# Kernel optimization log

Measured on AMD Instinct MI355X. Metric: run time of the kernel, lower is better.

Reference implementation:

```python
import jax, jax.numpy as jnp
import numpy as np

B, C, T_TEXT, T_FEAT = 32, 256, 512, 2048
DELTA = 0.1  # self.temperature


def setup_inputs() -> dict:
    key = jax.random.key(0)
    k1, k2 = jax.random.split(key)
    x = jax.random.normal(k1, (B, C, T_TEXT), dtype=jnp.float32)
    # token durations in frames, ~U[0, 8): avg ~4 frames/token -> T_FEAT ~ 2048
    w = jax.random.uniform(k2, (B, T_TEXT), dtype=jnp.float32) * 8.0
    x_mask = jnp.ones((B, T_TEXT), dtype=bool)
    y_mask = jnp.ones((B, T_FEAT), dtype=bool)
    return {"x": x, "w": w, "x_mask": x_mask, "y_mask": y_mask}


def reference(x, w, x_mask, y_mask):
    # Gaussian upsampling (arXiv 2010.04301) with fixed temperature DELTA.
    # x: (B, C, T_text), w: (B, T_text), x_mask: (B, T_text), y_mask: (B, T_feat)
    T_feats = y_mask.shape[-1]
    # frame time indices, zeroed where y_mask is False
    t = jnp.arange(T_feats, dtype=jnp.float32)[None, :] * y_mask.astype(jnp.float32)  # (B, T_feat)
    # Gaussian centers: cumulative duration minus half of own duration
    c = jnp.cumsum(w, axis=-1) - 0.5 * w  # (B, T_text)
    # energy: -delta * (t - c)^2  -> (B, T_feat, T_text)
    energy = -DELTA * (t[:, :, None] - c[:, None, :]) ** 2
    # mask out padded text tokens
    energy = jnp.where(x_mask[:, None, :], energy, -jnp.inf)
    p_attn = jax.nn.softmax(energy, axis=-1)  # (B, T_feat, T_text)
    # weighted sum over text tokens: (B, C, T_feat)
    out = jnp.einsum("btn,bcn->bct", p_attn, x)
    return out
```

## Files before the change

### kernel.cpp

```cpp
#include <hip/hip_runtime.h>
#include <hip/hip_bf16.h>

#define B_    32
#define C_    256
#define NT    512
#define TFEAT 2048
#define TT    32
#define UW    96
#define PRE   32
#define DELTA 0.1f
#define PSTR  104

typedef __attribute__((ext_vector_type(4))) float f32x4;
typedef __attribute__((ext_vector_type(8))) unsigned short u16x8;
typedef __attribute__((ext_vector_type(8))) __bf16 bf16x8;

static __device__ inline unsigned short f2bfbits(float f) {
    __bf16 h = (__bf16)f;
    return __builtin_bit_cast(unsigned short, h);
}
static __device__ inline float bf2f(unsigned short h) {
    return __uint_as_float(((unsigned)h) << 16);
}

__global__ __launch_bounds__(512) void centers_kernel(const float* __restrict__ w,
                                                      float* __restrict__ cout,
                                                      int* __restrict__ lotab) {
    int b = blockIdx.x;
    int tid = threadIdx.x;
    int lane = tid & 63, wv = tid >> 6;
    __shared__ float wsum[8];
    __shared__ float cs[NT];

    float wval = w[b * NT + tid];
    float s = wval;
#pragma unroll
    for (int off = 1; off < 64; off <<= 1) {
        float v = __shfl_up(s, off);
        if (lane >= off) s += v;
    }
    if (lane == 63) wsum[wv] = s;
    __syncthreads();
    float base = 0.f;
#pragma unroll
    for (int i = 0; i < 8; ++i) base += (i < wv) ? wsum[i] : 0.f;
    float c = base + s - 0.5f * wval;
    cs[tid] = c;
    cout[b * NT + tid] = c;
    __syncthreads();

    if (tid < TFEAT / TT) {
        float ft = (float)(tid * TT);
        int lo = 0, hi = NT;
        while (hi > lo) {
            int mid = (lo + hi) >> 1;
            if (cs[mid] < ft) lo = mid + 1; else hi = mid;
        }
        int n1 = lo < NT - 1 ? lo : NT - 1;
        int n0 = lo - 1 > 0 ? lo - 1 : 0;
        int nstar = (fabsf(ft - cs[n0]) <= fabsf(ft - cs[n1])) ? n0 : n1;
        int L = (nstar - PRE) & ~3;
        if (L < 0) L = 0;
        if (L > NT - UW) L = NT - UW;
        lotab[b * (TFEAT / TT) + tid] = L;
    }
}

__global__ __launch_bounds__(256) void fused_kernel(const float* __restrict__ x,
                                                    const float* __restrict__ cw,
                                                    const int* __restrict__ lotab,
                                                    float* __restrict__ out) {
    __shared__ unsigned short Pt[TT][PSTR];
    __shared__ float Sinv[TT];

    int tid = threadIdx.x;
    int bx  = blockIdx.x;
    int b    = bx & 31;
    int tile = bx >> 5;
    int t0   = tile * TT;
    int LO   = lotab[b * (TFEAT / TT) + tile];

    int wv   = tid >> 6;
    int lane = tid & 63;
    int arow = lane & 15;
    int kg   = lane >> 4;
    const float* xb = x + ((size_t)b * C_) * NT + LO + kg * 8;
    f32x4 areg[12][2];
#pragma unroll
    for (int m = 0; m < 4; ++m) {
        const float* xr = xb + (size_t)(wv * 64 + m * 16 + arow) * NT;
#pragma unroll
        for (int ks = 0; ks < 3; ++ks) {
            areg[m * 3 + ks][0] = *reinterpret_cast<const f32x4*>(xr + ks * 32);
            areg[m * 3 + ks][1] = *reinterpret_cast<const f32x4*>(xr + ks * 32 + 4);
        }
    }

    int g = tid >> 3;
    int j = tid & 7;
    float ft = (float)(t0 + g);

    float csv[12];
    const float* cp = cw + b * NT + LO + j;
#pragma unroll
    for (int k = 0; k < 12; ++k) csv[k] = cp[8 * k];

    float e[12];
    float mx = -1e30f;
#pragma unroll
    for (int k = 0; k < 12; ++k) {
        float d = ft - csv[k];
        e[k] = -DELTA * d * d;
        mx = fmaxf(mx, e[k]);
    }
    mx = fmaxf(mx, __shfl_xor(mx, 1));
    mx = fmaxf(mx, __shfl_xor(mx, 2));
    mx = fmaxf(mx, __shfl_xor(mx, 4));

    float sum = 0.f;
#pragma unroll
    for (int k = 0; k < 12; ++k) {
        unsigned short pb = f2bfbits(__expf(e[k] - mx));
        sum += bf2f(pb);
        Pt[g][j + 8 * k] = pb;
    }
    sum += __shfl_xor(sum, 1);
    sum += __shfl_xor(sum, 2);
    sum += __shfl_xor(sum, 4);
    if (j == 0) Sinv[g] = 1.f / fmaxf(sum, 1e-30f);

    bf16x8 afrag[12];
#pragma unroll
    for (int f = 0; f < 12; ++f) {
        bf16x8 v;
#pragma unroll
        for (int q = 0; q < 4; ++q) {
            v[q]     = (__bf16)areg[f][0][q];
            v[q + 4] = (__bf16)areg[f][1][q];
        }
        afrag[f] = v;
    }
    __syncthreads();

    bf16x8 bfrag[6];
#pragma unroll
    for (int nt = 0; nt < 2; ++nt)
#pragma unroll
        for (int ks = 0; ks < 3; ++ks) {
            const u16x8* p = reinterpret_cast<const u16x8*>(
                &Pt[nt * 16 + (lane & 15)][ks * 32 + kg * 8]);
            bfrag[nt * 3 + ks] = __builtin_bit_cast(bf16x8, *p);
        }

    f32x4 acc[4][2];
#pragma unroll
    for (int m = 0; m < 4; ++m)
#pragma unroll
        for (int nt = 0; nt < 2; ++nt)
            acc[m][nt] = (f32x4){0.f, 0.f, 0.f, 0.f};
#pragma unroll
    for (int m = 0; m < 4; ++m)
#pragma unroll
        for (int nt = 0; nt < 2; ++nt)
#pragma unroll
            for (int ks = 0; ks < 3; ++ks)
                acc[m][nt] = __builtin_amdgcn_mfma_f32_16x16x32_bf16(
                    afrag[m * 3 + ks], bfrag[nt * 3 + ks], acc[m][nt], 0, 0, 0);

    float si0 = Sinv[lane & 15];
    float si1 = Sinv[16 + (lane & 15)];
    int orow = (lane >> 4) * 4;
    float* ob = out + ((size_t)b * C_) * TFEAT + t0;
#pragma unroll
    for (int m = 0; m < 4; ++m) {
        int c = wv * 64 + m * 16 + orow;
#pragma unroll
        for (int r = 0; r < 4; ++r) {
            __builtin_nontemporal_store(acc[m][0][r] * si0,
                ob + (size_t)(c + r) * TFEAT + (lane & 15));
            __builtin_nontemporal_store(acc[m][1][r] * si1,
                ob + (size_t)(c + r) * TFEAT + 16 + (lane & 15));
        }
    }
}

extern "C" void kernel_launch(void* const* d_in, const int* in_sizes, int n_in,
                              void* d_out, int out_size, void* d_ws, size_t ws_size,
                              hipStream_t stream) {
    const float* x = (const float*)d_in[0];
    const float* w = (const float*)d_in[1];
    float* out  = (float*)d_out;
    float* cbuf = (float*)d_ws;
    int*   lotab = (int*)((char*)d_ws + 65536);

    hipLaunchKernelGGL(centers_kernel, dim3(B_), dim3(NT), 0, stream, w, cbuf, lotab);
    hipLaunchKernelGGL(fused_kernel, dim3(B_ * (TFEAT / TT)), dim3(256), 0, stream,
                       x, cbuf, lotab, out);
}
```

Baseline: 35.95 us.

## Fuse centers computation into main kernel and pipeline four tiles per block

Removes the separate centers/lotab kernel. Each block now recomputes the cumulative-sum centers for its batch in shared memory and finds the window starts with a ballot-based search. Each block then processes four time tiles with double-buffered softmax weights, prefetching the next tile's x window and softmax while storing the current one. This removes one launch and the global round trip for the centers, at the cost of a redundant prefix sum per block and fewer blocks (512 instead of 2048).

```diff
diff --git a/kernel.cpp b/kernel.cpp
--- a/kernel.cpp
+++ b/kernel.cpp
@@ -10,6 +10,8 @@
 #define PRE   32
 #define DELTA 0.1f
 #define PSTR  104
+#define TPB   4
+#define NGRP  16
 
 typedef __attribute__((ext_vector_type(4))) float f32x4;
 typedef __attribute__((ext_vector_type(8))) unsigned short u16x8;
@@ -23,163 +25,188 @@
     return __uint_as_float(((unsigned)h) << 16);
 }
 
-__global__ __launch_bounds__(512) void centers_kernel(const float* __restrict__ w,
-                                                      float* __restrict__ cout,
-                                                      int* __restrict__ lotab) {
-    int b = blockIdx.x;
-    int tid = threadIdx.x;
-    int lane = tid & 63, wv = tid >> 6;
+__global__ __launch_bounds__(256, 2) void fused_kernel(const float* __restrict__ x,
+                                                       const float* __restrict__ w,
+                                                       float* __restrict__ out) {
+    __shared__ float cs[NT];
     __shared__ float wsum[8];
-    __shared__ float cs[NT];
-
-    float wval = w[b * NT + tid];
-    float s = wval;
+    __shared__ unsigned short Pt[2][TT][PSTR];
+    __shared__ float Sinv[2][TT];
+    __shared__ int sLO[TPB];
+
+    int tid  = threadIdx.x;
+    int bx   = blockIdx.x;
+    int b    = bx & 31;
+    int grp  = bx >> 5;
+    int lane = tid & 63;
+    int wv   = tid >> 6;
+
+    float v0 = w[b * NT + tid];
+    float v1 = w[b * NT + 256 + tid];
+    float s0 = v0, s1 = v1;
 #pragma unroll
     for (int off = 1; off < 64; off <<= 1) {
-        float v = __shfl_up(s, off);
-        if (lane >= off) s += v;
+        float t0 = __shfl_up(s0, off);
+        float t1 = __shfl_up(s1, off);
+        if (lane >= off) { s0 += t0; s1 += t1; }
     }
-    if (lane == 63) wsum[wv] = s;
-    __syncthreads();
-    float base = 0.f;
-#pragma unroll
-    for (int i = 0; i < 8; ++i) base += (i < wv) ? wsum[i] : 0.f;
-    float c = base + s - 0.5f * wval;
-    cs[tid] = c;
-    cout[b * NT + tid] = c;
-    __syncthreads();
-
-    if (tid < TFEAT / TT) {
-        float ft = (float)(tid * TT);
-        int lo = 0, hi = NT;
-        while (hi > lo) {
-            int mid = (lo + hi) >> 1;
-            if (cs[mid] < ft) lo = mid + 1; else hi = mid;
-        }
-        int n1 = lo < NT - 1 ? lo : NT - 1;
-        int n0 = lo - 1 > 0 ? lo - 1 : 0;
-        int nstar = (fabsf(ft - cs[n0]) <= fabsf(ft - cs[n1])) ? n0 : n1;
-        int L = (nstar - PRE) & ~3;
-        if (L < 0) L = 0;
-        if (L > NT - UW) L = NT - UW;
-        lotab[b * (TFEAT / TT) + tid] = L;
+    if (lane == 63) { wsum[wv] = s0; wsum[4 + wv] = s1; }
+    __syncthreads();
+    float pre0 = 0.f;
+    float pre1 = wsum[0] + wsum[1] + wsum[2] + wsum[3];
+#pragma unroll
+    for (int i = 0; i < 4; ++i) if (i < wv) pre0 += wsum[i];
+#pragma unroll
+    for (int i = 0; i < 4; ++i) if (i < wv) pre1 += wsum[4 + i];
+    cs[tid]       = pre0 + s0 - 0.5f * v0;
+    cs[256 + tid] = pre1 + s1 - 0.5f * v1;
+    __syncthreads();
+
+    if (wv == 0) {
+        int gid = lane >> 4;
+        int k   = lane & 15;
+        float ft = (float)((grp * TPB + gid) * TT);
+        bool p = cs[32 * k + 31] < ft;
+        unsigned long long m = __ballot(p);
+        int K = __popcll((m >> (gid * 16)) & 0xFFFFull);
+        int n;
+        if (K >= 16) {
+            n = NT;
+        } else {
+            int base = 32 * K;
+            bool pa = cs[base + k] < ft;
+            bool pb = cs[base + 16 + k] < ft;
+            unsigned long long ma = __ballot(pa);
+            unsigned long long mb = __ballot(pb);
+            n = base + __popcll((ma >> (gid * 16)) & 0xFFFFull)
+                     + __popcll((mb >> (gid * 16)) & 0xFFFFull);
+        }
+        if (k == 0) {
+            int n1 = n < NT - 1 ? n : NT - 1;
+            int n0 = n - 1 > 0 ? n - 1 : 0;
+            int nstar = (fabsf(ft - cs[n0]) <= fabsf(ft - cs[n1])) ? n0 : n1;
+            int L = (nstar - PRE) & ~3;
+            if (L < 0) L = 0;
+            if (L > NT - UW) L = NT - UW;
+            sLO[gid] = L;
+        }
     }
-}
-
-__global__ __launch_bounds__(256) void fused_kernel(const float* __restrict__ x,
-                                                    const float* __restrict__ cw,
-                                                    const int* __restrict__ lotab,
-                                                    float* __restrict__ out) {
-    __shared__ unsigned short Pt[TT][PSTR];
-    __shared__ float Sinv[TT];
-
-    int tid = threadIdx.x;
-    int bx  = blockIdx.x;
-    int b    = bx & 31;
-    int tile = bx >> 5;
-    int t0   = tile * TT;
-    int LO   = lotab[b * (TFEAT / TT) + tile];
-
-    int wv   = tid >> 6;
-    int lane = tid & 63;
-    int arow = lane & 15;
-    int kg   = lane >> 4;
-    const float* xb = x + ((size_t)b * C_) * NT + LO + kg * 8;
+    __syncthreads();
+
+    int g = tid >> 3, j = tid & 7;
+    int arow = lane & 15, kg = lane >> 4;
+
     f32x4 areg[12][2];
-#pragma unroll
-    for (int m = 0; m < 4; ++m) {
-        const float* xr = xb + (size_t)(wv * 64 + m * 16 + arow) * NT;
-#pragma unroll
-        for (int ks = 0; ks < 3; ++ks) {
-            areg[m * 3 + ks][0] = *reinterpret_cast<const f32x4*>(xr + ks * 32);
-            areg[m * 3 + ks][1] = *reinterpret_cast<const f32x4*>(xr + ks * 32 + 4);
-        }
-    }
-
-    int g = tid >> 3;
-    int j = tid & 7;
-    float ft = (float)(t0 + g);
-
-    float csv[12];
-    const float* cp = cw + b * NT + LO + j;
-#pragma unroll
-    for (int k = 0; k < 12; ++k) csv[k] = cp[8 * k];
-
-    float e[12];
-    float mx = -1e30f;
-#pragma unroll
-    for (int k = 0; k < 12; ++k) {
-        float d = ft - csv[k];
-        e[k] = -DELTA * d * d;
-        mx = fmaxf(mx, e[k]);
-    }
-    mx = fmaxf(mx, __shfl_xor(mx, 1));
-    mx = fmaxf(mx, __shfl_xor(mx, 2));
-    mx = fmaxf(mx, __shfl_xor(mx, 4));
-
-    float sum = 0.f;
-#pragma unroll
-    for (int k = 0; k < 12; ++k) {
-        unsigned short pb = f2bfbits(__expf(e[k] - mx));
-        sum += bf2f(pb);
-        Pt[g][j + 8 * k] = pb;
-    }
-    sum += __shfl_xor(sum, 1);
-    sum += __shfl_xor(sum, 2);
-    sum += __shfl_xor(sum, 4);
-    if (j == 0) Sinv[g] = 1.f / fmaxf(sum, 1e-30f);
-
-    bf16x8 afrag[12];
-#pragma unroll
-    for (int f = 0; f < 12; ++f) {
-        bf16x8 v;
-#pragma unroll
-        for (int q = 0; q < 4; ++q) {
-            v[q]     = (__bf16)areg[f][0][q];
-            v[q + 4] = (__bf16)areg[f][1][q];
-        }
-        afrag[f] = v;
-    }
-    __syncthreads();
-
-    bf16x8 bfrag[6];
-#pragma unroll
-    for (int nt = 0; nt < 2; ++nt)
-#pragma unroll
-        for (int ks = 0; ks < 3; ++ks) {
-            const u16x8* p = reinterpret_cast<const u16x8*>(
-                &Pt[nt * 16 + (lane & 15)][ks * 32 + kg * 8]);
-            bfrag[nt * 3 + ks] = __builtin_bit_cast(bf16x8, *p);
-        }
-
-    f32x4 acc[4][2];
-#pragma unroll
-    for (int m = 0; m < 4; ++m)
-#pragma unroll
-        for (int nt = 0; nt < 2; ++nt)
-            acc[m][nt] = (f32x4){0.f, 0.f, 0.f, 0.f};
-#pragma unroll
-    for (int m = 0; m < 4; ++m)
-#pragma unroll
-        for (int nt = 0; nt < 2; ++nt)
+
+    auto issue_A = [&](int it) {
+        int LO = sLO[it];
+        const float* xb = x + ((size_t)b * C_) * NT + LO + kg * 8;
+#pragma unroll
+        for (int m = 0; m < 4; ++m) {
+            const float* xr = xb + (size_t)(wv * 64 + m * 16 + arow) * NT;
+#pragma unroll
+            for (int ks = 0; ks < 3; ++ks) {
+                areg[m * 3 + ks][0] = *reinterpret_cast<const f32x4*>(xr + ks * 32);
+                areg[m * 3 + ks][1] = *reinterpret_cast<const f32x4*>(xr + ks * 32 + 4);
+            }
+        }
+    };
+
+    auto softmax_tile = [&](int it, int bf) {
+        int LO = sLO[it];
+        float ft = (float)((grp * TPB + it) * TT + g);
+        float e[12];
+        float mx = -1e30f;
+#pragma unroll
+        for (int k = 0; k < 12; ++k) {
+            float d = ft - cs[LO + j + 8 * k];
+            e[k] = -DELTA * d * d;
+            mx = fmaxf(mx, e[k]);
+        }
+        mx = fmaxf(mx, __shfl_xor(mx, 1));
+        mx = fmaxf(mx, __shfl_xor(mx, 2));
+        mx = fmaxf(mx, __shfl_xor(mx, 4));
+        float sum = 0.f;
+#pragma unroll
+        for (int k = 0; k < 12; ++k) {
+            unsigned short pbv = f2bfbits(__expf(e[k] - mx));
+            sum += bf2f(pbv);
+            Pt[bf][g][j + 8 * k] = pbv;
+        }
+        sum += __shfl_xor(sum, 1);
+        sum += __shfl_xor(sum, 2);
+        sum += __shfl_xor(sum, 4);
+        if (j == 0) Sinv[bf][g] = 1.f / fmaxf(sum, 1e-30f);
+    };
+
+    issue_A(0);
+    __builtin_amdgcn_sched_barrier(0);
+    softmax_tile(0, 0);
+    __syncthreads();
+
+    for (int it = 0; it < TPB; ++it) {
+        int bf = it & 1;
+
+        bf16x8 bfrag[6];
+#pragma unroll
+        for (int nt2 = 0; nt2 < 2; ++nt2)
 #pragma unroll
             for (int ks = 0; ks < 3; ++ks)
-                acc[m][nt] = __builtin_amdgcn_mfma_f32_16x16x32_bf16(
-                    afrag[m * 3 + ks], bfrag[nt * 3 + ks], acc[m][nt], 0, 0, 0);
-
-    float si0 = Sinv[lane & 15];
-    float si1 = Sinv[16 + (lane & 15)];
-    int orow = (lane >> 4) * 4;
-    float* ob = out + ((size_t)b * C_) * TFEAT + t0;
-#pragma unroll
-    for (int m = 0; m < 4; ++m) {
-        int c = wv * 64 + m * 16 + orow;
-#pragma unroll
-        for (int r = 0; r < 4; ++r) {
-            __builtin_nontemporal_store(acc[m][0][r] * si0,
-                ob + (size_t)(c + r) * TFEAT + (lane & 15));
-            __builtin_nontemporal_store(acc[m][1][r] * si1,
-                ob + (size_t)(c + r) * TFEAT + 16 + (lane & 15));
+                bfrag[nt2 * 3 + ks] = __builtin_bit_cast(bf16x8,
+                    *reinterpret_cast<const u16x8*>(
+                        &Pt[bf][nt2 * 16 + arow][ks * 32 + kg * 8]));
+
+        f32x4 acc[4][2];
+#pragma unroll
+        for (int m = 0; m < 4; ++m)
+#pragma unroll
+            for (int nt2 = 0; nt2 < 2; ++nt2)
+                acc[m][nt2] = (f32x4){0.f, 0.f, 0.f, 0.f};
+
+#pragma unroll
+        for (int m = 0; m < 4; ++m) {
+            bf16x8 af[3];
+#pragma unroll
+            for (int ks = 0; ks < 3; ++ks) {
+                bf16x8 vv;
+#pragma unroll
+                for (int q = 0; q < 4; ++q) {
+                    vv[q]     = (__bf16)areg[m * 3 + ks][0][q];
+                    vv[q + 4] = (__bf16)areg[m * 3 + ks][1][q];
+                }
+                af[ks] = vv;
+            }
+#pragma unroll
+            for (int nt2 = 0; nt2 < 2; ++nt2)
+#pragma unroll
+                for (int ks = 0; ks < 3; ++ks)
+                    acc[m][nt2] = __builtin_amdgcn_mfma_f32_16x16x32_bf16(
+                        af[ks], bfrag[nt2 * 3 + ks], acc[m][nt2], 0, 0, 0);
+        }
+
+        float si0 = Sinv[bf][arow];
+        float si1 = Sinv[bf][16 + arow];
+
+        if (it < TPB - 1) {
+            issue_A(it + 1);
+            __builtin_amdgcn_sched_barrier(0);
+            softmax_tile(it + 1, bf ^ 1);
+        }
+        __syncthreads();
+
+        int t0 = (grp * TPB + it) * TT;
+        float* ob = out + ((size_t)b * C_) * TFEAT + t0;
+        int orow = kg * 4;
+#pragma unroll
+        for (int m = 0; m < 4; ++m) {
+            int c = wv * 64 + m * 16 + orow;
+#pragma unroll
+            for (int r = 0; r < 4; ++r) {
+                __builtin_nontemporal_store(acc[m][0][r] * si0,
+                    ob + (size_t)(c + r) * TFEAT + arow);
+                __builtin_nontemporal_store(acc[m][1][r] * si1,
+                    ob + (size_t)(c + r) * TFEAT + 16 + arow);
+            }
         }
     }
 }
@@ -189,11 +216,8 @@
                               hipStream_t stream) {
     const float* x = (const float*)d_in[0];
     const float* w = (const float*)d_in[1];
-    float* out  = (float*)d_out;
-    float* cbuf = (float*)d_ws;
-    int*   lotab = (int*)((char*)d_ws + 65536);
-
-    hipLaunchKernelGGL(centers_kernel, dim3(B_), dim3(NT), 0, stream, w, cbuf, lotab);
-    hipLaunchKernelGGL(fused_kernel, dim3(B_ * (TFEAT / TT)), dim3(256), 0, stream,
-                       x, cbuf, lotab, out);
-}
+    float* out = (float*)d_out;
+
+    hipLaunchKernelGGL(fused_kernel, dim3(B_ * NGRP), dim3(256), 0, stream,
+                       x, w, out);
+}
```

Result: no change. 35.81 us (-0.4%).

## Restructure main kernel to single-wave blocks with register-resident softmax weights

Applied to the files above, without the earlier changes.

The main kernel now runs one 64-lane wave per block instead of four. Each lane computes the softmax weights directly in MFMA operand layout, so the shared-memory staging buffer and the barrier are gone. The wave then loops over all 256 channels in 16-row chunks, streaming x and writing 16-byte vector stores with the MFMA operands swapped. The prep kernel now runs 256 threads that each handle two elements of the cumsum. The cost is that each block carries more serial work and has less latency hiding from parallel waves, relying instead on the larger block count for occupancy.

```diff
diff --git a/kernel.cpp b/kernel.cpp
--- a/kernel.cpp
+++ b/kernel.cpp
@@ -9,7 +9,6 @@
 #define UW    96
 #define PRE   32
 #define DELTA 0.1f
-#define PSTR  104
 
 typedef __attribute__((ext_vector_type(4))) float f32x4;
 typedef __attribute__((ext_vector_type(8))) unsigned short u16x8;
@@ -23,30 +22,39 @@
     return __uint_as_float(((unsigned)h) << 16);
 }
 
-__global__ __launch_bounds__(512) void centers_kernel(const float* __restrict__ w,
-                                                      float* __restrict__ cout,
-                                                      int* __restrict__ lotab) {
-    int b = blockIdx.x;
-    int tid = threadIdx.x;
-    int lane = tid & 63, wv = tid >> 6;
+__global__ __launch_bounds__(256) void prep_kernel(const float* __restrict__ w,
+                                                   float* __restrict__ cout,
+                                                   int* __restrict__ lotab) {
+    __shared__ float cs[NT];
     __shared__ float wsum[8];
-    __shared__ float cs[NT];
+    int tid  = threadIdx.x;
+    int b    = blockIdx.x;
+    int lane = tid & 63;
+    int wv   = tid >> 6;
 
-    float wval = w[b * NT + tid];
-    float s = wval;
+    float v0 = w[b * NT + tid];
+    float v1 = w[b * NT + 256 + tid];
+    float s0 = v0, s1 = v1;
 #pragma unroll
     for (int off = 1; off < 64; off <<= 1) {
-        float v = __shfl_up(s, off);
-        if (lane >= off) s += v;
+        float t0 = __shfl_up(s0, off);
+        float t1 = __shfl_up(s1, off);
+        if (lane >= off) { s0 += t0; s1 += t1; }
     }
-    if (lane == 63) wsum[wv] = s;
+    if (lane == 63) { wsum[wv] = s0; wsum[4 + wv] = s1; }
     __syncthreads();
-    float base = 0.f;
+    float pre0 = 0.f;
+    float pre1 = wsum[0] + wsum[1] + wsum[2] + wsum[3];
 #pragma unroll
-    for (int i = 0; i < 8; ++i) base += (i < wv) ? wsum[i] : 0.f;
-    float c = base + s - 0.5f * wval;
-    cs[tid] = c;
-    cout[b * NT + tid] = c;
+    for (int i = 0; i < 4; ++i) if (i < wv) pre0 += wsum[i];
+#pragma unroll
+    for (int i = 0; i < 4; ++i) if (i < wv) pre1 += wsum[4 + i];
+    float c0 = pre0 + s0 - 0.5f * v0;
+    float c1 = pre1 + s1 - 0.5f * v1;
+    cs[tid]       = c0;
+    cs[256 + tid] = c1;
+    cout[b * NT + tid]       = c0;
+    cout[b * NT + 256 + tid] = c1;
     __syncthreads();
 
     if (tid < TFEAT / TT) {
@@ -66,121 +74,99 @@
     }
 }
 
-__global__ __launch_bounds__(256) void fused_kernel(const float* __restrict__ x,
-                                                    const float* __restrict__ cw,
-                                                    const int* __restrict__ lotab,
-                                                    float* __restrict__ out) {
-    __shared__ unsigned short Pt[TT][PSTR];
-    __shared__ float Sinv[TT];
-
-    int tid = threadIdx.x;
-    int bx  = blockIdx.x;
+__global__ __launch_bounds__(64) void g_kernel(const float* __restrict__ x,
+                                               const float* __restrict__ cw,
+                                               const int* __restrict__ lotab,
+                                               float* __restrict__ out) {
+    int bx   = blockIdx.x;
     int b    = bx & 31;
     int tile = bx >> 5;
+    int l    = threadIdx.x;
+    int fr   = l & 15;
+    int kg   = l >> 4;
+    int LO   = lotab[b * (TFEAT / TT) + tile];
     int t0   = tile * TT;
-    int LO   = lotab[b * (TFEAT / TT) + tile];
 
-    int wv   = tid >> 6;
-    int lane = tid & 63;
-    int arow = lane & 15;
-    int kg   = lane >> 4;
-    const float* xb = x + ((size_t)b * C_) * NT + LO + kg * 8;
-    f32x4 areg[12][2];
+    const float* cp = cw + b * NT + LO + kg * 8;
+    f32x4 cv[6];
 #pragma unroll
-    for (int m = 0; m < 4; ++m) {
-        const float* xr = xb + (size_t)(wv * 64 + m * 16 + arow) * NT;
+    for (int ks = 0; ks < 3; ++ks) {
+        cv[2 * ks]     = *reinterpret_cast<const f32x4*>(cp + ks * 32);
+        cv[2 * ks + 1] = *reinterpret_cast<const f32x4*>(cp + ks * 32 + 4);
+    }
+
+    float ft0 = (float)(t0 + fr);
+    float ft1 = (float)(t0 + 16 + fr);
+    float e0[24], e1[24];
+    float mx0 = -1e30f, mx1 = -1e30f;
+#pragma unroll
+    for (int ks = 0; ks < 3; ++ks)
+#pragma unroll
+        for (int q = 0; q < 8; ++q) {
+            float c = cv[2 * ks + (q >> 2)][q & 3];
+            float d0 = ft0 - c, d1 = ft1 - c;
+            float a0 = -DELTA * d0 * d0;
+            float a1 = -DELTA * d1 * d1;
+            e0[ks * 8 + q] = a0; mx0 = fmaxf(mx0, a0);
+            e1[ks * 8 + q] = a1; mx1 = fmaxf(mx1, a1);
+        }
+    mx0 = fmaxf(mx0, __shfl_xor(mx0, 16)); mx0 = fmaxf(mx0, __shfl_xor(mx0, 32));
+    mx1 = fmaxf(mx1, __shfl_xor(mx1, 16)); mx1 = fmaxf(mx1, __shfl_xor(mx1, 32));
+
+    bf16x8 af0[3], af1[3];
+    float sum0 = 0.f, sum1 = 0.f;
+#pragma unroll
+    for (int ks = 0; ks < 3; ++ks)
+#pragma unroll
+        for (int q = 0; q < 8; ++q) {
+            unsigned short p0 = f2bfbits(__expf(e0[ks * 8 + q] - mx0));
+            unsigned short p1 = f2bfbits(__expf(e1[ks * 8 + q] - mx1));
+            sum0 += bf2f(p0);
+            sum1 += bf2f(p1);
+            af0[ks][q] = __builtin_bit_cast(__bf16, p0);
+            af1[ks][q] = __builtin_bit_cast(__bf16, p1);
+        }
+    sum0 += __shfl_xor(sum0, 16); sum0 += __shfl_xor(sum0, 32);
+    sum1 += __shfl_xor(sum1, 16); sum1 += __shfl_xor(sum1, 32);
+    float inv0 = 1.f / fmaxf(sum0, 1e-30f);
+    float inv1 = 1.f / fmaxf(sum1, 1e-30f);
+
+    f32x4 sv0, sv1;
+#pragma unroll
+    for (int r = 0; r < 4; ++r) {
+        sv0[r] = __shfl(inv0, kg * 4 + r);
+        sv1[r] = __shfl(inv1, kg * 4 + r);
+    }
+
+    const float* xbase = x + ((size_t)b * C_) * NT + LO + kg * 8;
+    float* ob = out + ((size_t)b * C_) * TFEAT + t0 + kg * 4;
+
+#pragma unroll 2
+    for (int ct = 0; ct < 16; ++ct) {
+        const float* xr = xbase + (size_t)(ct * 16 + fr) * NT;
+        bf16x8 bfr[3];
 #pragma unroll
         for (int ks = 0; ks < 3; ++ks) {
-            areg[m * 3 + ks][0] = *reinterpret_cast<const f32x4*>(xr + ks * 32);
-            areg[m * 3 + ks][1] = *reinterpret_cast<const f32x4*>(xr + ks * 32 + 4);
+            f32x4 a0 = *reinterpret_cast<const f32x4*>(xr + ks * 32);
+            f32x4 a1 = *reinterpret_cast<const f32x4*>(xr + ks * 32 + 4);
+            bf16x8 vv;
+#pragma unroll
+            for (int q = 0; q < 4; ++q) {
+                vv[q]     = (__bf16)a0[q];
+                vv[q + 4] = (__bf16)a1[q];
+            }
+            bfr[ks] = vv;
         }
-    }
-
-    int g = tid >> 3;
-    int j = tid & 7;
-    float ft = (float)(t0 + g);
-
-    float csv[12];
-    const float* cp = cw + b * NT + LO + j;
-#pragma unroll
-    for (int k = 0; k < 12; ++k) csv[k] = cp[8 * k];
-
-    float e[12];
-    float mx = -1e30f;
-#pragma unroll
-    for (int k = 0; k < 12; ++k) {
-        float d = ft - csv[k];
-        e[k] = -DELTA * d * d;
-        mx = fmaxf(mx, e[k]);
-    }
-    mx = fmaxf(mx, __shfl_xor(mx, 1));
-    mx = fmaxf(mx, __shfl_xor(mx, 2));
-    mx = fmaxf(mx, __shfl_xor(mx, 4));
-
-    float sum = 0.f;
-#pragma unroll
-    for (int k = 0; k < 12; ++k) {
-        unsigned short pb = f2bfbits(__expf(e[k] - mx));
-        sum += bf2f(pb);
-        Pt[g][j + 8 * k] = pb;
-    }
-    sum += __shfl_xor(sum, 1);
-    sum += __shfl_xor(sum, 2);
-    sum += __shfl_xor(sum, 4);
-    if (j == 0) Sinv[g] = 1.f / fmaxf(sum, 1e-30f);
-
-    bf16x8 afrag[12];
-#pragma unroll
-    for (int f = 0; f < 12; ++f) {
-        bf16x8 v;
-#pragma unroll
-        for (int q = 0; q < 4; ++q) {
-            v[q]     = (__bf16)areg[f][0][q];
-            v[q + 4] = (__bf16)areg[f][1][q];
-        }
-        afrag[f] = v;
-    }
-    __syncthreads();
-
-    bf16x8 bfrag[6];
-#pragma unroll
-    for (int nt = 0; nt < 2; ++nt)
+        f32x4 acc0 = (f32x4){0.f, 0.f, 0.f, 0.f};
+        f32x4 acc1 = (f32x4){0.f, 0.f, 0.f, 0.f};
 #pragma unroll
         for (int ks = 0; ks < 3; ++ks) {
-            const u16x8* p = reinterpret_cast<const u16x8*>(
-                &Pt[nt * 16 + (lane & 15)][ks * 32 + kg * 8]);
-            bfrag[nt * 3 + ks] = __builtin_bit_cast(bf16x8, *p);
+            acc0 = __builtin_amdgcn_mfma_f32_16x16x32_bf16(af0[ks], bfr[ks], acc0, 0, 0, 0);
+            acc1 = __builtin_amdgcn_mfma_f32_16x16x32_bf16(af1[ks], bfr[ks], acc1, 0, 0, 0);
         }
-
-    f32x4 acc[4][2];
-#pragma unroll
-    for (int m = 0; m < 4; ++m)
-#pragma unroll
-        for (int nt = 0; nt < 2; ++nt)
-            acc[m][nt] = (f32x4){0.f, 0.f, 0.f, 0.f};
-#pragma unroll
-    for (int m = 0; m < 4; ++m)
-#pragma unroll
-        for (int nt = 0; nt < 2; ++nt)
-#pragma unroll
-            for (int ks = 0; ks < 3; ++ks)
-                acc[m][nt] = __builtin_amdgcn_mfma_f32_16x16x32_bf16(
-                    afrag[m * 3 + ks], bfrag[nt * 3 + ks], acc[m][nt], 0, 0, 0);
-
-    float si0 = Sinv[lane & 15];
-    float si1 = Sinv[16 + (lane & 15)];
-    int orow = (lane >> 4) * 4;
-    float* ob = out + ((size_t)b * C_) * TFEAT + t0;
-#pragma unroll
-    for (int m = 0; m < 4; ++m) {
-        int c = wv * 64 + m * 16 + orow;
-#pragma unroll
-        for (int r = 0; r < 4; ++r) {
-            __builtin_nontemporal_store(acc[m][0][r] * si0,
-                ob + (size_t)(c + r) * TFEAT + (lane & 15));
-            __builtin_nontemporal_store(acc[m][1][r] * si1,
-                ob + (size_t)(c + r) * TFEAT + 16 + (lane & 15));
-        }
+        float* op = ob + (size_t)(ct * 16 + fr) * TFEAT;
+        __builtin_nontemporal_store(acc0 * sv0, reinterpret_cast<f32x4*>(op));
+        __builtin_nontemporal_store(acc1 * sv1, reinterpret_cast<f32x4*>(op + 16));
     }
 }
 
@@ -193,7 +179,7 @@
     float* cbuf = (float*)d_ws;
     int*   lotab = (int*)((char*)d_ws + 65536);
 
-    hipLaunchKernelGGL(centers_kernel, dim3(B_), dim3(NT), 0, stream, w, cbuf, lotab);
-    hipLaunchKernelGGL(fused_kernel, dim3(B_ * (TFEAT / TT)), dim3(256), 0, stream,
+    hipLaunchKernelGGL(prep_kernel, dim3(B_), dim3(256), 0, stream, w, cbuf, lotab);
+    hipLaunchKernelGGL(g_kernel, dim3(B_ * (TFEAT / TT)), dim3(64), 0, stream,
                        x, cbuf, lotab, out);
 }
```

Result: no change. 36.38 us (+1.2%).
